# Kernel tuning notes

Measured on AMD Instinct MI355X. Metric: run time of the kernel, lower is better.

The kernel has to match this reference:

```python
import jax, jax.numpy as jnp
import numpy as np

N = 100000      # nodes
E = 1600000     # edges
F_IN = 64       # num_features
H = 64          # hidden_channels
NG = 64         # graphs in batch
ALPHA = 0.5


def _lin_init(key, fan_in, fan_out):
    kw, kb = jax.random.split(key)
    bound = 1.0 / np.sqrt(fan_in)
    w = jax.random.uniform(kw, (fan_in, fan_out), jnp.float32, -bound, bound)
    b = jax.random.uniform(kb, (fan_out,), jnp.float32, -bound, bound)
    return w, b


def setup_inputs() -> dict:
    key = jax.random.key(0)
    ks = jax.random.split(key, 12)
    x = jax.random.normal(ks[0], (N, F_IN), dtype=jnp.float32)
    edge_index = jax.random.randint(ks[1], (2, E), 0, N, dtype=jnp.int32)
    batch = jnp.sort(jax.random.randint(ks[2], (N,), 0, NG, dtype=jnp.int32))
    w1s, b1s = _lin_init(ks[3], F_IN, H)
    w1d, b1d = _lin_init(ks[4], F_IN, H)
    w2s, b2s = _lin_init(ks[5], H, H)
    w2d, b2d = _lin_init(ks[6], H, H)
    w3s, b3s = _lin_init(ks[7], H, H)
    w3d, b3d = _lin_init(ks[8], H, H)
    wl1, bl1 = _lin_init(ks[9], H, 5)
    wl2, bl2 = _lin_init(ks[10], 5, 1)
    return dict(x=x, edge_index=edge_index, batch=batch,
                w1s=w1s, b1s=b1s, w1d=w1d, b1d=b1d,
                w2s=w2s, b2s=b2s, w2d=w2d, b2d=b2d,
                w3s=w3s, b3s=b3s, w3d=w3d, b3d=b3d,
                wl1=wl1, bl1=bl1, wl2=wl2, bl2=bl2)


def _dir_gcn_conv(x, row, col, ws, bs, wd, bd):
    # directional norm: D_out^{-1/2} A D_in^{-1/2} (and same recipe for A^T)
    ones = jnp.ones((row.shape[0],), x.dtype)
    deg_out = jax.ops.segment_sum(ones, row, num_segments=N)  # row-sums of A
    deg_in = jax.ops.segment_sum(ones, col, num_segments=N)   # col-sums of A
    r_out = jnp.where(deg_out > 0, deg_out ** -0.5, 0.0)
    r_in = jnp.where(deg_in > 0, deg_in ** -0.5, 0.0)
    norm = r_out[row] * r_in[col]  # per-edge weight; identical for A and A^T norms
    msg = norm[:, None] * x[col]                       # [E, F]
    adj_x = jax.ops.segment_sum(msg, row, num_segments=N)
    msg_t = norm[:, None] * x[row]
    adj_t_x = jax.ops.segment_sum(msg_t, col, num_segments=N)
    return ALPHA * (adj_x @ ws + bs) + (1.0 - ALPHA) * (adj_t_x @ wd + bd)


def reference(x, edge_index, batch,
              w1s, b1s, w1d, b1d,
              w2s, b2s, w2d, b2d,
              w3s, b3s, w3d, b3d,
              wl1, bl1, wl2, bl2):
    row, col = edge_index[0], edge_index[1]
    h = jax.nn.relu(_dir_gcn_conv(x, row, col, w1s, b1s, w1d, b1d))
    h = jax.nn.relu(_dir_gcn_conv(h, row, col, w2s, b2s, w2d, b2d))
    h = jax.nn.relu(_dir_gcn_conv(h, row, col, w3s, b3s, w3d, b3d))
    g = jax.ops.segment_max(h, batch, num_segments=NG)  # global max pool [NG, H]
    g = jax.nn.relu(g @ wl1 + bl1)
    return g @ wl2 + bl2  # [NG, 1]
```

## Files before the change

### kernel.cpp

```cpp
#include <hip/hip_runtime.h>

#define N_NODES 100000
#define N_EDGES 1600000
#define EPAD    (N_EDGES + NB * BW)
#define HDIM    64
#define NGRAPH  64
#define BW      256
#define NB      391
#define NBLK    256
#define CHUNK   ((N_EDGES + NBLK - 1) / NBLK)
#define MTILES  (N_NODES / 16)

typedef _Float16 h16;
typedef _Float16 h16x4 __attribute__((ext_vector_type(4)));
typedef _Float16 h16x8 __attribute__((ext_vector_type(8)));
typedef float    f32x4 __attribute__((ext_vector_type(4)));

__global__ __launch_bounds__(512) void bucket_count(const int* __restrict__ ei,
                                                    int* __restrict__ cntTabA,
                                                    int* __restrict__ cntTabT) {
    __shared__ int cA[NB], cT[NB];
    const int tid = threadIdx.x;
    for (int i = tid; i < NB; i += 512) { cA[i] = 0; cT[i] = 0; }
    __syncthreads();
    const int e0 = blockIdx.x * CHUNK, e1 = min(e0 + CHUNK, N_EDGES);
    for (int e = e0 + tid; e < e1; e += 512) {
        int r = ei[e];
        int c = ei[N_EDGES + e];
        atomicAdd(&cA[r >> 8], 1);
        atomicAdd(&cT[c >> 8], 1);
    }
    __syncthreads();
    for (int b = tid; b < NB; b += 512) {
        cntTabA[b * NBLK + blockIdx.x] = cA[b];
        cntTabT[b * NBLK + blockIdx.x] = cT[b];
    }
}

__global__ __launch_bounds__(256) void chunk_scan(int* __restrict__ cntTabA,
                                                  int* __restrict__ cntTabT,
                                                  int* __restrict__ tot) {
    __shared__ int s[256];
    const int b = blockIdx.x, d = blockIdx.y, tid = threadIdx.x;
    int* tab = d ? cntTabT : cntTabA;
    int v = tab[b * NBLK + tid];
    s[tid] = v;
    __syncthreads();
    for (int off = 1; off < 256; off <<= 1) {
        int t = (tid >= off) ? s[tid - off] : 0;
        __syncthreads();
        s[tid] += t;
        __syncthreads();
    }
    tab[b * NBLK + tid] = s[tid] - v;
    if (tid == 255) tot[d * 512 + b] = s[255];
}

__global__ __launch_bounds__(512) void start_scan(const int* __restrict__ tot,
                                                  int* __restrict__ bktStartA,
                                                  int* __restrict__ bktStartT) {
    __shared__ int s[512];
    const int tid = threadIdx.x;
    int v = (tid < NB) ? tot[tid] : 0;
    s[tid] = v;
    __syncthreads();
    for (int off = 1; off < 512; off <<= 1) {
        int t = (tid >= off) ? s[tid - off] : 0;
        __syncthreads();
        s[tid] += t;
        __syncthreads();
    }
    if (tid < NB) bktStartA[tid] = s[tid] - v;
    if (tid == 0) bktStartA[NB] = N_EDGES;
    __syncthreads();
    int v2 = (tid < NB) ? tot[512 + tid] : 0;
    s[tid] = v2;
    __syncthreads();
    for (int off = 1; off < 512; off <<= 1) {
        int t = (tid >= off) ? s[tid - off] : 0;
        __syncthreads();
        s[tid] += t;
        __syncthreads();
    }
    if (tid < NB) bktStartT[tid] = s[tid] - v2;
    if (tid == 0) bktStartT[NB] = N_EDGES;
}

__global__ __launch_bounds__(512) void bucketize_write(const int* __restrict__ ei,
                                                       const int* __restrict__ cntTabA,
                                                       const int* __restrict__ cntTabT,
                                                       const int* __restrict__ bktStartA,
                                                       const int* __restrict__ bktStartT,
                                                       int2* __restrict__ bktA,
                                                       int2* __restrict__ bktT) {
    __shared__ int bA[NB], bT[NB];
    const int tid = threadIdx.x;
    for (int i = tid; i < NB; i += 512) {
        bA[i] = bktStartA[i] + cntTabA[i * NBLK + blockIdx.x];
        bT[i] = bktStartT[i] + cntTabT[i * NBLK + blockIdx.x];
    }
    __syncthreads();
    const int e0 = blockIdx.x * CHUNK, e1 = min(e0 + CHUNK, N_EDGES);
    for (int e = e0 + tid; e < e1; e += 512) {
        int r = ei[e];
        int c = ei[N_EDGES + e];
        int pA = atomicAdd(&bA[r >> 8], 1);
        bktA[pA] = make_int2(r, c);
        int pT = atomicAdd(&bT[c >> 8], 1);
        bktT[pT] = make_int2(c, r);
    }
}

__global__ __launch_bounds__(256) void bucket_deg_ptr(
        const int* __restrict__ bktStartA, const int* __restrict__ bktStartT,
        const int2* __restrict__ bktA, const int2* __restrict__ bktT,
        int* __restrict__ deg_out, int* __restrict__ deg_in,
        float* __restrict__ r_out, float* __restrict__ r_in,
        int* __restrict__ rowptrP, int* __restrict__ colptrP) {
    __shared__ int c[BW];
    __shared__ int s[256];
    const int b = blockIdx.x, d = blockIdx.y, tid = threadIdx.x;
    const int* bs = d ? bktStartT : bktStartA;
    const int2* bkt = d ? bktT : bktA;
    int* deg = d ? deg_in : deg_out;
    float* rr = d ? r_in : r_out;
    int* ptr = d ? colptrP : rowptrP;
    const int node0 = b * BW;
    c[tid] = 0;
    __syncthreads();
    const int i0 = bs[b], i1 = bs[b + 1];
    for (int i = i0 + tid; i < i1; i += 256) atomicAdd(&c[bkt[i].x - node0], 1);
    __syncthreads();
    int n = node0 + tid, dg = c[tid];
    int pad = dg + (dg & 1);
    if (n < N_NODES) {
        deg[n] = dg;
        rr[n] = dg > 0 ? rsqrtf((float)dg) : 0.0f;
    } else pad = 0;
    s[tid] = pad;
    __syncthreads();
    for (int off = 1; off < 256; off <<= 1) {
        int t = (tid >= off) ? s[tid - off] : 0;
        __syncthreads();
        s[tid] += t;
        __syncthreads();
    }
    if (n < N_NODES) ptr[n] = i0 + b * BW + (s[tid] - pad);
}

__global__ __launch_bounds__(512) void bucket_scatter(
        const int* __restrict__ rowptrP, const int* __restrict__ colptrP,
        const float* __restrict__ r_out, const float* __restrict__ r_in,
        const int* __restrict__ bktStartA, const int* __restrict__ bktStartT,
        const int2* __restrict__ bktA, const int2* __restrict__ bktT,
        int2* __restrict__ recA, int2* __restrict__ recT) {
    __shared__ int cur[BW];
    __shared__ float rwt[BW];
    const int b = blockIdx.x, d = blockIdx.y, tid = threadIdx.x;
    const int* ptr = d ? colptrP : rowptrP;
    const float* rt = d ? r_in : r_out;
    const float* rs = d ? r_out : r_in;
    const int* bs = d ? bktStartT : bktStartA;
    const int2* bkt = d ? bktT : bktA;
    int2* rec = d ? recT : recA;
    const int node0 = b * BW;
    if (tid < BW) {
        int n = node0 + tid;
        cur[tid] = (n < N_NODES) ? ptr[n] : 0;
        rwt[tid] = (n < N_NODES) ? rt[n] : 0.0f;
    }
    __syncthreads();
    const int i0 = bs[b], i1 = bs[b + 1];
    for (int i = i0 + tid; i < i1; i += 512) {
        int2 e = bkt[i];
        float w = rwt[e.x - node0] * rs[e.y];
        int p = atomicAdd(&cur[e.x - node0], 1);
        rec[p] = make_int2(e.y << 7, __float_as_int(w));
    }
}

__global__ __launch_bounds__(256) void cast_kernel(const float4* __restrict__ x,
                                                   h16x4* __restrict__ xh,
                                                   unsigned* __restrict__ g) {
    if (blockIdx.x == 0) {
        for (int j = threadIdx.x; j < NGRAPH * HDIM; j += 256) g[j] = 0u;
    }
    int i = blockIdx.x * 256 + threadIdx.x;
    if (i < N_NODES * 16) {
        float4 v = x[i];
        h16x4 o;
        o.x = (h16)v.x; o.y = (h16)v.y; o.z = (h16)v.z; o.w = (h16)v.w;
        xh[i] = o;
    }
}

__global__ __launch_bounds__(256) void wprep_kernel(
        const float* __restrict__ w1s, const float* __restrict__ w1d,
        const float* __restrict__ w2s, const float* __restrict__ w2d,
        const float* __restrict__ w3s, const float* __restrict__ w3d,
        const float* __restrict__ b1s, const float* __restrict__ b1d,
        const float* __restrict__ b2s, const float* __restrict__ b2d,
        const float* __restrict__ b3s, const float* __restrict__ b3d,
        h16* __restrict__ WT, float* __restrict__ bc) {
    const int l = blockIdx.y;
    const float* ws = l == 0 ? w1s : l == 1 ? w2s : w3s;
    const float* wd = l == 0 ? w1d : l == 1 ? w2d : w3d;
    int e = blockIdx.x * 256 + threadIdx.x;
    if (e < 8192) {
        int f = e >> 7, k = e & 127;
        float v = (k < 64) ? ws[k * 64 + f] : wd[(k - 64) * 64 + f];
        WT[l * 8192 + f * 128 + k] = (h16)(0.5f * v);
    }
    if (blockIdx.x == 0 && threadIdx.x < 64) {
        const float* bs = l == 0 ? b1s : l == 1 ? b2s : b3s;
        const float* bd = l == 0 ? b1d : l == 1 ? b2d : b3d;
        bc[l * 64 + threadIdx.x] = 0.5f * (bs[threadIdx.x] + bd[threadIdx.x]);
    }
}

__device__ __forceinline__ void fma4h(float4& a, float w, h16x4 f) {
    a.x = fmaf(w, (float)f.x, a.x);
    a.y = fmaf(w, (float)f.y, a.y);
    a.z = fmaf(w, (float)f.z, a.z);
    a.w = fmaf(w, (float)f.w, a.w);
}

__device__ __forceinline__ float4 red_s(float4 v) {
    v.x += __shfl_xor(v.x, 16); v.y += __shfl_xor(v.y, 16);
    v.z += __shfl_xor(v.z, 16); v.w += __shfl_xor(v.w, 16);
    v.x += __shfl_xor(v.x, 32); v.y += __shfl_xor(v.y, 32);
    v.z += __shfl_xor(v.z, 32); v.w += __shfl_xor(v.w, 32);
    return v;
}

__device__ __forceinline__ h16x4 ld_h4(const char* __restrict__ p) {
    return *(const h16x4*)p;
}

__device__ __forceinline__ float4 agg_dir(const char* __restrict__ hb,
                                          const int2* __restrict__ rec,
                                          int start, int deg, int q, int s, int sh) {
    float4 a0 = {0.f,0.f,0.f,0.f}, a1 = {0.f,0.f,0.f,0.f};
    float4 a2 = {0.f,0.f,0.f,0.f}, a3 = {0.f,0.f,0.f,0.f};
    const int4* rec4 = (const int4*)(rec + start);
    const int qb = q * 8;
    int k = 0;
    for (; k + 16 <= deg; k += 16) {
        int4 p0 = rec4[(k >> 1) + s];
        int4 p1 = rec4[(k >> 1) + 4 + s];
        h16x4 f0 = ld_h4(hb + (p0.x << sh) + qb);
        h16x4 f1 = ld_h4(hb + (p0.z << sh) + qb);
        h16x4 f2 = ld_h4(hb + (p1.x << sh) + qb);
        h16x4 f3 = ld_h4(hb + (p1.z << sh) + qb);
        fma4h(a0, __int_as_float(p0.y), f0);
        fma4h(a1, __int_as_float(p0.w), f1);
        fma4h(a2, __int_as_float(p1.y), f2);
        fma4h(a3, __int_as_float(p1.w), f3);
    }
    if (k + 8 <= deg) {
        int4 p = rec4[(k >> 1) + s];
        h16x4 f0 = ld_h4(hb + (p.x << sh) + qb);
        h16x4 f1 = ld_h4(hb + (p.z << sh) + qb);
        fma4h(a0, __int_as_float(p.y), f0);
        fma4h(a1, __int_as_float(p.w), f1);
        k += 8;
    }
    int r = deg - k;
    if (2 * s < r) {
        int4 p = rec4[(k >> 1) + s];
        h16x4 f0 = ld_h4(hb + (p.x << sh) + qb);
        fma4h(a2, __int_as_float(p.y), f0);
        if (2 * s + 1 < r) {
            h16x4 f1 = ld_h4(hb + (p.z << sh) + qb);
            fma4h(a3, __int_as_float(p.w), f1);
        }
    }
    a0.x += a1.x; a0.y += a1.y; a0.z += a1.z; a0.w += a1.w;
    a2.x += a3.x; a2.y += a3.y; a2.z += a3.z; a2.w += a3.w;
    a0.x += a2.x; a0.y += a2.y; a0.z += a2.z; a0.w += a2.w;
    return red_s(a0);
}

__global__ __launch_bounds__(256) void agg_kernel(
        const char* __restrict__ h_in, char* __restrict__ acc_out, int sh,
        const int* __restrict__ rowptrP, const int* __restrict__ deg_out,
        const int2* __restrict__ recA,
        const int* __restrict__ colptrP, const int* __restrict__ deg_in,
        const int2* __restrict__ recT) {
    const int tid  = threadIdx.x;
    const int wid  = (blockIdx.x << 2) + (tid >> 6);
    const int lane = tid & 63;
    const int node = wid >> 1;
    const int dir  = wid & 1;
    const int q = lane & 15;
    const int s = lane >> 4;

    const int* ptr = dir ? colptrP : rowptrP;
    const int* deg = dir ? deg_in : deg_out;
    const int2* rec = dir ? recT : recA;

    float4 a = agg_dir(h_in, rec, ptr[node], deg[node], q, s, sh);
    if (s == 0) {
        h16x4 pk;
        pk.x = (h16)a.x; pk.y = (h16)a.y; pk.z = (h16)a.z; pk.w = (h16)a.w;
        *(h16x4*)(acc_out + (size_t)node * 256 + dir * 128 + q * 8) = pk;
    }
}

__global__ __launch_bounds__(256) void gemm_kernel(char* __restrict__ acc,
                                                   const h16* __restrict__ WT,
                                                   const float* __restrict__ bc,
                                                   const int* __restrict__ batch,
                                                   unsigned* __restrict__ g,
                                                   int do_pool) {
    const int lane = threadIdx.x & 63;
    const int wid = (blockIdx.x * 256 + threadIdx.x) >> 6;
    const int nW = gridDim.x * 4;
    const int m = lane & 15, t = lane >> 4;

    h16x8 bfrag[4][4];
    float bb[4];
#pragma unroll
    for (int nt = 0; nt < 4; nt++) {
        bb[nt] = bc[nt * 16 + m];
#pragma unroll
        for (int kk = 0; kk < 4; kk++)
            bfrag[nt][kk] = *(const h16x8*)(WT + (nt * 16 + m) * 128 + kk * 32 + t * 8);
    }

    for (int tile = wid; tile < MTILES; tile += nW) {
        char* arow = acc + (size_t)tile * 16 * 256;
        const int node0 = tile * 16;
        int b0 = 0, b15 = 0;
        if (do_pool) { b0 = batch[node0]; b15 = batch[node0 + 15]; }
        h16x8 afrag[4];
#pragma unroll
        for (int kk = 0; kk < 4; kk++)
            afrag[kk] = *(const h16x8*)(arow + m * 256 + kk * 64 + t * 16);
#pragma unroll
        for (int nt = 0; nt < 4; nt++) {
            f32x4 c = {0.f, 0.f, 0.f, 0.f};
#pragma unroll
            for (int kk = 0; kk < 4; kk++)
                c = __builtin_amdgcn_mfma_f32_16x16x32_f16(afrag[kk], bfrag[nt][kk], c, 0, 0, 0);
            float ov[4];
#pragma unroll
            for (int r = 0; r < 4; r++) {
                ov[r] = fmaxf(c[r] + bb[nt], 0.0f);
                *(h16*)(arow + (t * 4 + r) * 256 + (nt * 16 + m) * 2) = (h16)ov[r];
            }
            if (do_pool) {
                if (b0 == b15) {
                    float mx = fmaxf(fmaxf(ov[0], ov[1]), fmaxf(ov[2], ov[3]));
                    mx = fmaxf(mx, __shfl_xor(mx, 16));
                    mx = fmaxf(mx, __shfl_xor(mx, 32));
                    if (t == 0)
                        atomicMax(&g[b0 * HDIM + nt * 16 + m], __float_as_uint(mx));
                } else {
#pragma unroll
                    for (int r = 0; r < 4; r++)
                        atomicMax(&g[batch[node0 + t * 4 + r] * HDIM + nt * 16 + m],
                                  __float_as_uint(ov[r]));
                }
            }
        }
    }
}

__global__ __launch_bounds__(64) void mlp_kernel(const unsigned* __restrict__ g,
                                                 const float* __restrict__ wl1,
                                                 const float* __restrict__ bl1,
                                                 const float* __restrict__ wl2,
                                                 const float* __restrict__ bl2,
                                                 float* __restrict__ out) {
    int t = threadIdx.x;
    float gv[HDIM];
#pragma unroll
    for (int k = 0; k < HDIM; k++) gv[k] = __uint_as_float(g[t * HDIM + k]);
    float o = bl2[0];
#pragma unroll
    for (int j = 0; j < 5; j++) {
        float hj = bl1[j];
#pragma unroll
        for (int k = 0; k < HDIM; k++) hj += gv[k] * wl1[k * 5 + j];
        hj = fmaxf(hj, 0.0f);
        o += hj * wl2[j];
    }
    out[t] = o;
}

extern "C" void kernel_launch(void* const* d_in, const int* in_sizes, int n_in,
                              void* d_out, int out_size, void* d_ws, size_t ws_size,
                              hipStream_t stream) {
    const float* x   = (const float*)d_in[0];
    const int*   ei  = (const int*)d_in[1];
    const int*   bat = (const int*)d_in[2];
    const float* w1s = (const float*)d_in[3];
    const float* b1s = (const float*)d_in[4];
    const float* w1d = (const float*)d_in[5];
    const float* b1d = (const float*)d_in[6];
    const float* w2s = (const float*)d_in[7];
    const float* b2s = (const float*)d_in[8];
    const float* w2d = (const float*)d_in[9];
    const float* b2d = (const float*)d_in[10];
    const float* w3s = (const float*)d_in[11];
    const float* b3s = (const float*)d_in[12];
    const float* w3d = (const float*)d_in[13];
    const float* b3d = (const float*)d_in[14];
    const float* wl1 = (const float*)d_in[15];
    const float* bl1 = (const float*)d_in[16];
    const float* wl2 = (const float*)d_in[17];
    const float* bl2 = (const float*)d_in[18];
    float* out = (float*)d_out;

    char* p = (char*)d_ws;
    int*   deg_out = (int*)p;              p += N_NODES * 4;
    int*   deg_in  = (int*)p;              p += N_NODES * 4;
    int*   rowptrP = (int*)p;              p += N_NODES * 4;
    int*   colptrP = (int*)p;              p += N_NODES * 4;
    float* r_out   = (float*)p;            p += N_NODES * 4;
    float* r_in    = (float*)p;            p += N_NODES * 4;
    int*   cntTabA = (int*)p;              p += (size_t)NB * NBLK * 4;
    int*   cntTabT = (int*)p;              p += (size_t)NB * NBLK * 4;
    int*   totTab  = (int*)p;              p += 1024 * 4;
    int*   bktStartA = (int*)p;            p += 512 * 4;
    int*   bktStartT = (int*)p;            p += 512 * 4;
    int2*  recA    = (int2*)p;             p += (size_t)EPAD * 8;
    int2*  recT    = (int2*)p;             p += (size_t)EPAD * 8;
    char*  bufP    = p;
    int2*  bktA    = (int2*)p;
    int2*  bktT    = (int2*)(p + (size_t)N_EDGES * 8);
    p += 2 * (size_t)N_EDGES * 8;
    char*  bufQ    = p;
    h16*   xh      = (h16*)p;
    p += 2 * (size_t)N_EDGES * 8;
    unsigned* g    = (unsigned*)p;         p += NGRAPH * HDIM * 4;
    h16*   WT      = (h16*)p;              p += 3 * 8192 * 2;
    float* bc      = (float*)p;            p += 3 * 64 * 4;

    cast_kernel<<<(N_NODES * 16 + 255) / 256, 256, 0, stream>>>(
        (const float4*)x, (h16x4*)xh, g);
    dim3 gw(32, 3);
    wprep_kernel<<<gw, 256, 0, stream>>>(w1s, w1d, w2s, w2d, w3s, w3d,
                                         b1s, b1d, b2s, b2d, b3s, b3d, WT, bc);

    bucket_count<<<NBLK, 512, 0, stream>>>(ei, cntTabA, cntTabT);
    dim3 gb2(NB, 2);
    chunk_scan<<<gb2, 256, 0, stream>>>(cntTabA, cntTabT, totTab);
    start_scan<<<1, 512, 0, stream>>>(totTab, bktStartA, bktStartT);
    bucketize_write<<<NBLK, 512, 0, stream>>>(ei, cntTabA, cntTabT,
                                              bktStartA, bktStartT, bktA, bktT);

    dim3 gb(NB, 2);
    bucket_deg_ptr<<<gb, 256, 0, stream>>>(bktStartA, bktStartT, bktA, bktT,
                                           deg_out, deg_in, r_out, r_in,
                                           rowptrP, colptrP);
    bucket_scatter<<<gb, 512, 0, stream>>>(
        rowptrP, colptrP, r_out, r_in, bktStartA, bktStartT, bktA, bktT, recA, recT);

    const int agrid = N_NODES * 2 / 4;
    agg_kernel<<<agrid, 256, 0, stream>>>((const char*)xh, bufP, 0,
                                          rowptrP, deg_out, recA, colptrP, deg_in, recT);
    gemm_kernel<<<256, 256, 0, stream>>>(bufP, WT, bc, bat, g, 0);
    agg_kernel<<<agrid, 256, 0, stream>>>(bufP, bufQ, 1,
                                          rowptrP, deg_out, recA, colptrP, deg_in, recT);
    gemm_kernel<<<256, 256, 0, stream>>>(bufQ, WT + 8192, bc + 64, bat, g, 0);
    agg_kernel<<<agrid, 256, 0, stream>>>(bufQ, bufP, 1,
                                          rowptrP, deg_out, recA, colptrP, deg_in, recT);
    gemm_kernel<<<256, 256, 0, stream>>>(bufP, WT + 16384, bc + 128, bat, g, 1);

    mlp_kernel<<<1, 64, 0, stream>>>(g, wl1, bl1, wl2, bl2, out);
}
```

Before: 489.0 us.

## Factor edge norm into node scaling and shrink edge records to one int

The per-edge weight r_out[row]*r_in[col] is split into per-node factors. Source features are prescaled by r_in or r_out when they are written (in cast and in the GEMM epilogue), and the destination factor is applied after aggregation. Edge records shrink from an int2 (index plus weight) to a single pre-shifted byte offset, and the degree and scatter kernels are merged into one launch. This roughly halves index traffic in the gather loops and removes the multiplies. In exchange the feature buffers now store two prescaled copies, padding grows to multiples of 4, and the GEMM writes two half-precision copies per output.

```diff
diff --git a/kernel.cpp b/kernel.cpp
--- a/kernel.cpp
+++ b/kernel.cpp
@@ -2,11 +2,12 @@
 
 #define N_NODES 100000
 #define N_EDGES 1600000
-#define EPAD    (N_EDGES + NB * BW)
+#define BW      256
+#define NB      391
+#define SLACK   (3 * BW)
+#define EPAD    (N_EDGES + NB * SLACK)
 #define HDIM    64
 #define NGRAPH  64
-#define BW      256
-#define NB      391
 #define NBLK    256
 #define CHUNK   ((N_EDGES + NBLK - 1) / NBLK)
 #define MTILES  (N_NODES / 16)
@@ -111,20 +112,23 @@
     }
 }
 
-__global__ __launch_bounds__(256) void bucket_deg_ptr(
+__global__ __launch_bounds__(256) void deg_scatter(
         const int* __restrict__ bktStartA, const int* __restrict__ bktStartT,
         const int2* __restrict__ bktA, const int2* __restrict__ bktT,
         int* __restrict__ deg_out, int* __restrict__ deg_in,
         float* __restrict__ r_out, float* __restrict__ r_in,
-        int* __restrict__ rowptrP, int* __restrict__ colptrP) {
+        int* __restrict__ rowptrP, int* __restrict__ colptrP,
+        int* __restrict__ recA, int* __restrict__ recT) {
     __shared__ int c[BW];
     __shared__ int s[256];
+    __shared__ int cur[BW];
     const int b = blockIdx.x, d = blockIdx.y, tid = threadIdx.x;
     const int* bs = d ? bktStartT : bktStartA;
     const int2* bkt = d ? bktT : bktA;
     int* deg = d ? deg_in : deg_out;
     float* rr = d ? r_in : r_out;
     int* ptr = d ? colptrP : rowptrP;
+    int* rec = d ? recT : recA;
     const int node0 = b * BW;
     c[tid] = 0;
     __syncthreads();
@@ -132,65 +136,52 @@
     for (int i = i0 + tid; i < i1; i += 256) atomicAdd(&c[bkt[i].x - node0], 1);
     __syncthreads();
     int n = node0 + tid, dg = c[tid];
-    int pad = dg + (dg & 1);
+    int pad = (dg + 3) & ~3;
+    if (n >= N_NODES) pad = 0;
+    s[tid] = pad;
+    __syncthreads();
+    for (int off = 1; off < 256; off <<= 1) {
+        int t = (tid >= off) ? s[tid - off] : 0;
+        __syncthreads();
+        s[tid] += t;
+        __syncthreads();
+    }
+    int my_ptr = i0 + SLACK * b + (s[tid] - pad);
     if (n < N_NODES) {
         deg[n] = dg;
         rr[n] = dg > 0 ? rsqrtf((float)dg) : 0.0f;
-    } else pad = 0;
-    s[tid] = pad;
-    __syncthreads();
-    for (int off = 1; off < 256; off <<= 1) {
-        int t = (tid >= off) ? s[tid - off] : 0;
-        __syncthreads();
-        s[tid] += t;
-        __syncthreads();
-    }
-    if (n < N_NODES) ptr[n] = i0 + b * BW + (s[tid] - pad);
-}
-
-__global__ __launch_bounds__(512) void bucket_scatter(
-        const int* __restrict__ rowptrP, const int* __restrict__ colptrP,
-        const float* __restrict__ r_out, const float* __restrict__ r_in,
-        const int* __restrict__ bktStartA, const int* __restrict__ bktStartT,
-        const int2* __restrict__ bktA, const int2* __restrict__ bktT,
-        int2* __restrict__ recA, int2* __restrict__ recT) {
-    __shared__ int cur[BW];
-    __shared__ float rwt[BW];
-    const int b = blockIdx.x, d = blockIdx.y, tid = threadIdx.x;
-    const int* ptr = d ? colptrP : rowptrP;
-    const float* rt = d ? r_in : r_out;
-    const float* rs = d ? r_out : r_in;
-    const int* bs = d ? bktStartT : bktStartA;
-    const int2* bkt = d ? bktT : bktA;
-    int2* rec = d ? recT : recA;
-    const int node0 = b * BW;
-    if (tid < BW) {
-        int n = node0 + tid;
-        cur[tid] = (n < N_NODES) ? ptr[n] : 0;
-        rwt[tid] = (n < N_NODES) ? rt[n] : 0.0f;
-    }
-    __syncthreads();
-    const int i0 = bs[b], i1 = bs[b + 1];
-    for (int i = i0 + tid; i < i1; i += 512) {
+        ptr[n] = my_ptr;
+    }
+    cur[tid] = my_ptr;
+    __syncthreads();
+    for (int i = i0 + tid; i < i1; i += 256) {
         int2 e = bkt[i];
-        float w = rwt[e.x - node0] * rs[e.y];
         int p = atomicAdd(&cur[e.x - node0], 1);
-        rec[p] = make_int2(e.y << 7, __float_as_int(w));
+        rec[p] = e.y << 8;
     }
 }
 
 __global__ __launch_bounds__(256) void cast_kernel(const float4* __restrict__ x,
-                                                   h16x4* __restrict__ xh,
+                                                   const float* __restrict__ r_in,
+                                                   const float* __restrict__ r_out,
+                                                   char* __restrict__ xh,
                                                    unsigned* __restrict__ g) {
     if (blockIdx.x == 0) {
         for (int j = threadIdx.x; j < NGRAPH * HDIM; j += 256) g[j] = 0u;
     }
     int i = blockIdx.x * 256 + threadIdx.x;
     if (i < N_NODES * 16) {
+        int node = i >> 4, q = i & 15;
         float4 v = x[i];
-        h16x4 o;
-        o.x = (h16)v.x; o.y = (h16)v.y; o.z = (h16)v.z; o.w = (h16)v.w;
-        xh[i] = o;
+        float ri = r_in[node], ro = r_out[node];
+        h16x4 a, t;
+        a.x = (h16)(v.x * ri); a.y = (h16)(v.y * ri);
+        a.z = (h16)(v.z * ri); a.w = (h16)(v.w * ri);
+        t.x = (h16)(v.x * ro); t.y = (h16)(v.y * ro);
+        t.z = (h16)(v.z * ro); t.w = (h16)(v.w * ro);
+        char* row = xh + (size_t)node * 256;
+        *(h16x4*)(row + q * 8) = a;
+        *(h16x4*)(row + 128 + q * 8) = t;
     }
 }
 
@@ -218,11 +209,9 @@
     }
 }
 
-__device__ __forceinline__ void fma4h(float4& a, float w, h16x4 f) {
-    a.x = fmaf(w, (float)f.x, a.x);
-    a.y = fmaf(w, (float)f.y, a.y);
-    a.z = fmaf(w, (float)f.z, a.z);
-    a.w = fmaf(w, (float)f.w, a.w);
+__device__ __forceinline__ void add4h(float4& a, h16x4 f) {
+    a.x += (float)f.x; a.y += (float)f.y;
+    a.z += (float)f.z; a.w += (float)f.w;
 }
 
 __device__ __forceinline__ float4 red_s(float4 v) {
@@ -238,42 +227,31 @@
 }
 
 __device__ __forceinline__ float4 agg_dir(const char* __restrict__ hb,
-                                          const int2* __restrict__ rec,
-                                          int start, int deg, int q, int s, int sh) {
+                                          const int* __restrict__ rec,
+                                          int start, int deg, int qb, int s) {
     float4 a0 = {0.f,0.f,0.f,0.f}, a1 = {0.f,0.f,0.f,0.f};
     float4 a2 = {0.f,0.f,0.f,0.f}, a3 = {0.f,0.f,0.f,0.f};
     const int4* rec4 = (const int4*)(rec + start);
-    const int qb = q * 8;
     int k = 0;
     for (; k + 16 <= deg; k += 16) {
-        int4 p0 = rec4[(k >> 1) + s];
-        int4 p1 = rec4[(k >> 1) + 4 + s];
-        h16x4 f0 = ld_h4(hb + (p0.x << sh) + qb);
-        h16x4 f1 = ld_h4(hb + (p0.z << sh) + qb);
-        h16x4 f2 = ld_h4(hb + (p1.x << sh) + qb);
-        h16x4 f3 = ld_h4(hb + (p1.z << sh) + qb);
-        fma4h(a0, __int_as_float(p0.y), f0);
-        fma4h(a1, __int_as_float(p0.w), f1);
-        fma4h(a2, __int_as_float(p1.y), f2);
-        fma4h(a3, __int_as_float(p1.w), f3);
-    }
-    if (k + 8 <= deg) {
-        int4 p = rec4[(k >> 1) + s];
-        h16x4 f0 = ld_h4(hb + (p.x << sh) + qb);
-        h16x4 f1 = ld_h4(hb + (p.z << sh) + qb);
-        fma4h(a0, __int_as_float(p.y), f0);
-        fma4h(a1, __int_as_float(p.w), f1);
-        k += 8;
+        int4 p = rec4[(k >> 2) + s];
+        h16x4 f0 = ld_h4(hb + p.x + qb);
+        h16x4 f1 = ld_h4(hb + p.y + qb);
+        h16x4 f2 = ld_h4(hb + p.z + qb);
+        h16x4 f3 = ld_h4(hb + p.w + qb);
+        add4h(a0, f0);
+        add4h(a1, f1);
+        add4h(a2, f2);
+        add4h(a3, f3);
     }
     int r = deg - k;
-    if (2 * s < r) {
-        int4 p = rec4[(k >> 1) + s];
-        h16x4 f0 = ld_h4(hb + (p.x << sh) + qb);
-        fma4h(a2, __int_as_float(p.y), f0);
-        if (2 * s + 1 < r) {
-            h16x4 f1 = ld_h4(hb + (p.z << sh) + qb);
-            fma4h(a3, __int_as_float(p.w), f1);
-        }
+    int base = 4 * s;
+    if (base < r) {
+        int4 p = rec4[(k >> 2) + s];
+        add4h(a0, ld_h4(hb + p.x + qb));
+        if (base + 1 < r) add4h(a1, ld_h4(hb + p.y + qb));
+        if (base + 2 < r) add4h(a2, ld_h4(hb + p.z + qb));
+        if (base + 3 < r) add4h(a3, ld_h4(hb + p.w + qb));
     }
     a0.x += a1.x; a0.y += a1.y; a0.z += a1.z; a0.w += a1.w;
     a2.x += a3.x; a2.y += a3.y; a2.z += a3.z; a2.w += a3.w;
@@ -282,11 +260,12 @@
 }
 
 __global__ __launch_bounds__(256) void agg_kernel(
-        const char* __restrict__ h_in, char* __restrict__ acc_out, int sh,
+        const char* __restrict__ h_in, char* __restrict__ acc_out,
         const int* __restrict__ rowptrP, const int* __restrict__ deg_out,
-        const int2* __restrict__ recA,
+        const int* __restrict__ recA,
         const int* __restrict__ colptrP, const int* __restrict__ deg_in,
-        const int2* __restrict__ recT) {
+        const int* __restrict__ recT,
+        const float* __restrict__ r_out, const float* __restrict__ r_in) {
     const int tid  = threadIdx.x;
     const int wid  = (blockIdx.x << 2) + (tid >> 6);
     const int lane = tid & 63;
@@ -297,12 +276,16 @@
 
     const int* ptr = dir ? colptrP : rowptrP;
     const int* deg = dir ? deg_in : deg_out;
-    const int2* rec = dir ? recT : recA;
-
-    float4 a = agg_dir(h_in, rec, ptr[node], deg[node], q, s, sh);
+    const int* rec = dir ? recT : recA;
+    const float* rt = dir ? r_in : r_out;
+    const int qb = dir * 128 + q * 8;
+
+    float4 a = agg_dir(h_in, rec, ptr[node], deg[node], qb, s);
     if (s == 0) {
+        float sc = rt[node];
         h16x4 pk;
-        pk.x = (h16)a.x; pk.y = (h16)a.y; pk.z = (h16)a.z; pk.w = (h16)a.w;
+        pk.x = (h16)(a.x * sc); pk.y = (h16)(a.y * sc);
+        pk.z = (h16)(a.z * sc); pk.w = (h16)(a.w * sc);
         *(h16x4*)(acc_out + (size_t)node * 256 + dir * 128 + q * 8) = pk;
     }
 }
@@ -310,6 +293,8 @@
 __global__ __launch_bounds__(256) void gemm_kernel(char* __restrict__ acc,
                                                    const h16* __restrict__ WT,
                                                    const float* __restrict__ bc,
+                                                   const float* __restrict__ r_in,
+                                                   const float* __restrict__ r_out,
                                                    const int* __restrict__ batch,
                                                    unsigned* __restrict__ g,
                                                    int do_pool) {
@@ -332,7 +317,16 @@
         char* arow = acc + (size_t)tile * 16 * 256;
         const int node0 = tile * 16;
         int b0 = 0, b15 = 0;
-        if (do_pool) { b0 = batch[node0]; b15 = batch[node0 + 15]; }
+        float ri[4], ro[4];
+        if (do_pool) {
+            b0 = batch[node0]; b15 = batch[node0 + 15];
+        } else {
+#pragma unroll
+            for (int r = 0; r < 4; r++) {
+                ri[r] = r_in[node0 + t * 4 + r];
+                ro[r] = r_out[node0 + t * 4 + r];
+            }
+        }
         h16x8 afrag[4];
 #pragma unroll
         for (int kk = 0; kk < 4; kk++)
@@ -345,10 +339,8 @@
                 c = __builtin_amdgcn_mfma_f32_16x16x32_f16(afrag[kk], bfrag[nt][kk], c, 0, 0, 0);
             float ov[4];
 #pragma unroll
-            for (int r = 0; r < 4; r++) {
+            for (int r = 0; r < 4; r++)
                 ov[r] = fmaxf(c[r] + bb[nt], 0.0f);
-                *(h16*)(arow + (t * 4 + r) * 256 + (nt * 16 + m) * 2) = (h16)ov[r];
-            }
             if (do_pool) {
                 if (b0 == b15) {
                     float mx = fmaxf(fmaxf(ov[0], ov[1]), fmaxf(ov[2], ov[3]));
@@ -361,6 +353,13 @@
                     for (int r = 0; r < 4; r++)
                         atomicMax(&g[batch[node0 + t * 4 + r] * HDIM + nt * 16 + m],
                                   __float_as_uint(ov[r]));
+                }
+            } else {
+#pragma unroll
+                for (int r = 0; r < 4; r++) {
+                    char* rp = arow + (t * 4 + r) * 256 + (nt * 16 + m) * 2;
+                    *(h16*)rp = (h16)(ov[r] * ri[r]);
+                    *(h16*)(rp + 128) = (h16)(ov[r] * ro[r]);
                 }
             }
         }
@@ -425,21 +424,18 @@
     int*   totTab  = (int*)p;              p += 1024 * 4;
     int*   bktStartA = (int*)p;            p += 512 * 4;
     int*   bktStartT = (int*)p;            p += 512 * 4;
-    int2*  recA    = (int2*)p;             p += (size_t)EPAD * 8;
-    int2*  recT    = (int2*)p;             p += (size_t)EPAD * 8;
+    int*   recA    = (int*)p;              p += (size_t)EPAD * 4;
+    int*   recT    = (int*)p;              p += (size_t)EPAD * 4;
     char*  bufP    = p;
     int2*  bktA    = (int2*)p;
     int2*  bktT    = (int2*)(p + (size_t)N_EDGES * 8);
     p += 2 * (size_t)N_EDGES * 8;
     char*  bufQ    = p;
-    h16*   xh      = (h16*)p;
     p += 2 * (size_t)N_EDGES * 8;
     unsigned* g    = (unsigned*)p;         p += NGRAPH * HDIM * 4;
     h16*   WT      = (h16*)p;              p += 3 * 8192 * 2;
     float* bc      = (float*)p;            p += 3 * 64 * 4;
 
-    cast_kernel<<<(N_NODES * 16 + 255) / 256, 256, 0, stream>>>(
-        (const float4*)x, (h16x4*)xh, g);
     dim3 gw(32, 3);
     wprep_kernel<<<gw, 256, 0, stream>>>(w1s, w1d, w2s, w2d, w3s, w3d,
                                          b1s, b1d, b2s, b2d, b3s, b3d, WT, bc);
@@ -452,22 +448,26 @@
                                               bktStartA, bktStartT, bktA, bktT);
 
     dim3 gb(NB, 2);
-    bucket_deg_ptr<<<gb, 256, 0, stream>>>(bktStartA, bktStartT, bktA, bktT,
-                                           deg_out, deg_in, r_out, r_in,
-                                           rowptrP, colptrP);
-    bucket_scatter<<<gb, 512, 0, stream>>>(
-        rowptrP, colptrP, r_out, r_in, bktStartA, bktStartT, bktA, bktT, recA, recT);
+    deg_scatter<<<gb, 256, 0, stream>>>(bktStartA, bktStartT, bktA, bktT,
+                                        deg_out, deg_in, r_out, r_in,
+                                        rowptrP, colptrP, recA, recT);
+
+    cast_kernel<<<(N_NODES * 16 + 255) / 256, 256, 0, stream>>>(
+        (const float4*)x, r_in, r_out, bufQ, g);
 
     const int agrid = N_NODES * 2 / 4;
-    agg_kernel<<<agrid, 256, 0, stream>>>((const char*)xh, bufP, 0,
-                                          rowptrP, deg_out, recA, colptrP, deg_in, recT);
-    gemm_kernel<<<256, 256, 0, stream>>>(bufP, WT, bc, bat, g, 0);
-    agg_kernel<<<agrid, 256, 0, stream>>>(bufP, bufQ, 1,
-                                          rowptrP, deg_out, recA, colptrP, deg_in, recT);
-    gemm_kernel<<<256, 256, 0, stream>>>(bufQ, WT + 8192, bc + 64, bat, g, 0);
-    agg_kernel<<<agrid, 256, 0, stream>>>(bufQ, bufP, 1,
-                                          rowptrP, deg_out, recA, colptrP, deg_in, recT);
-    gemm_kernel<<<256, 256, 0, stream>>>(bufP, WT + 16384, bc + 128, bat, g, 1);
+    agg_kernel<<<agrid, 256, 0, stream>>>(bufQ, bufP,
+                                          rowptrP, deg_out, recA, colptrP, deg_in, recT,
+                                          r_out, r_in);
+    gemm_kernel<<<256, 256, 0, stream>>>(bufP, WT, bc, r_in, r_out, bat, g, 0);
+    agg_kernel<<<agrid, 256, 0, stream>>>(bufP, bufQ,
+                                          rowptrP, deg_out, recA, colptrP, deg_in, recT,
+                                          r_out, r_in);
+    gemm_kernel<<<256, 256, 0, stream>>>(bufQ, WT + 8192, bc + 64, r_in, r_out, bat, g, 0);
+    agg_kernel<<<agrid, 256, 0, stream>>>(bufQ, bufP,
+                                          rowptrP, deg_out, recA, colptrP, deg_in, recT,
+                                          r_out, r_in);
+    gemm_kernel<<<256, 256, 0, stream>>>(bufP, WT + 16384, bc + 128, r_in, r_out, bat, g, 1);
 
     mlp_kernel<<<1, 64, 0, stream>>>(g, wl1, bl1, wl2, bl2, out);
 }
```

Result: no change. 492.3 us (+0.7%).

## Fuse neighbor aggregation and MFMA linear layer into one kernel per layer

Applied to the files above, without the earlier changes.

Each GCN layer's gather-aggregate and its dense transform now run in one kernel. A 1024-thread block aggregates 8 nodes in both directions into shared memory, then four waves apply the 16x16x32 MFMA with bias and ReLU, writing a 128-byte fp16 row per node. This removes the round trip of the 256-byte aggregate buffer through global memory and the separate GEMM launch. In exchange, half the MFMA tile is wasted on 8-row groups, the weight fragments are reloaded in every block, and only 4 of 16 waves do the GEMM after a block-wide barrier.

```diff
diff --git a/kernel.cpp b/kernel.cpp
--- a/kernel.cpp
+++ b/kernel.cpp
@@ -9,7 +9,7 @@
 #define NB      391
 #define NBLK    256
 #define CHUNK   ((N_EDGES + NBLK - 1) / NBLK)
-#define MTILES  (N_NODES / 16)
+#define NGROUPS (N_NODES / 8)
 
 typedef _Float16 h16;
 typedef _Float16 h16x4 __attribute__((ext_vector_type(4)));
@@ -133,19 +133,20 @@
     __syncthreads();
     int n = node0 + tid, dg = c[tid];
     int pad = dg + (dg & 1);
+    if (n >= N_NODES) pad = 0;
+    s[tid] = pad;
+    __syncthreads();
+    for (int off = 1; off < 256; off <<= 1) {
+        int t = (tid >= off) ? s[tid - off] : 0;
+        __syncthreads();
+        s[tid] += t;
+        __syncthreads();
+    }
     if (n < N_NODES) {
         deg[n] = dg;
         rr[n] = dg > 0 ? rsqrtf((float)dg) : 0.0f;
-    } else pad = 0;
-    s[tid] = pad;
-    __syncthreads();
-    for (int off = 1; off < 256; off <<= 1) {
-        int t = (tid >= off) ? s[tid - off] : 0;
-        __syncthreads();
-        s[tid] += t;
-        __syncthreads();
-    }
-    if (n < N_NODES) ptr[n] = i0 + b * BW + (s[tid] - pad);
+        ptr[n] = i0 + b * BW + (s[tid] - pad);
+    }
 }
 
 __global__ __launch_bounds__(512) void bucket_scatter(
@@ -239,19 +240,18 @@
 
 __device__ __forceinline__ float4 agg_dir(const char* __restrict__ hb,
                                           const int2* __restrict__ rec,
-                                          int start, int deg, int q, int s, int sh) {
+                                          int start, int deg, int qb, int s) {
     float4 a0 = {0.f,0.f,0.f,0.f}, a1 = {0.f,0.f,0.f,0.f};
     float4 a2 = {0.f,0.f,0.f,0.f}, a3 = {0.f,0.f,0.f,0.f};
     const int4* rec4 = (const int4*)(rec + start);
-    const int qb = q * 8;
     int k = 0;
     for (; k + 16 <= deg; k += 16) {
         int4 p0 = rec4[(k >> 1) + s];
         int4 p1 = rec4[(k >> 1) + 4 + s];
-        h16x4 f0 = ld_h4(hb + (p0.x << sh) + qb);
-        h16x4 f1 = ld_h4(hb + (p0.z << sh) + qb);
-        h16x4 f2 = ld_h4(hb + (p1.x << sh) + qb);
-        h16x4 f3 = ld_h4(hb + (p1.z << sh) + qb);
+        h16x4 f0 = ld_h4(hb + p0.x + qb);
+        h16x4 f1 = ld_h4(hb + p0.z + qb);
+        h16x4 f2 = ld_h4(hb + p1.x + qb);
+        h16x4 f3 = ld_h4(hb + p1.z + qb);
         fma4h(a0, __int_as_float(p0.y), f0);
         fma4h(a1, __int_as_float(p0.w), f1);
         fma4h(a2, __int_as_float(p1.y), f2);
@@ -259,8 +259,8 @@
     }
     if (k + 8 <= deg) {
         int4 p = rec4[(k >> 1) + s];
-        h16x4 f0 = ld_h4(hb + (p.x << sh) + qb);
-        h16x4 f1 = ld_h4(hb + (p.z << sh) + qb);
+        h16x4 f0 = ld_h4(hb + p.x + qb);
+        h16x4 f1 = ld_h4(hb + p.z + qb);
         fma4h(a0, __int_as_float(p.y), f0);
         fma4h(a1, __int_as_float(p.w), f1);
         k += 8;
@@ -268,10 +268,10 @@
     int r = deg - k;
     if (2 * s < r) {
         int4 p = rec4[(k >> 1) + s];
-        h16x4 f0 = ld_h4(hb + (p.x << sh) + qb);
+        h16x4 f0 = ld_h4(hb + p.x + qb);
         fma4h(a2, __int_as_float(p.y), f0);
         if (2 * s + 1 < r) {
-            h16x4 f1 = ld_h4(hb + (p.z << sh) + qb);
+            h16x4 f1 = ld_h4(hb + p.z + qb);
             fma4h(a3, __int_as_float(p.w), f1);
         }
     }
@@ -281,17 +281,25 @@
     return red_s(a0);
 }
 
-__global__ __launch_bounds__(256) void agg_kernel(
-        const char* __restrict__ h_in, char* __restrict__ acc_out, int sh,
+#define ASTRIDE 132
+__global__ __launch_bounds__(1024) void layer_fused(
+        const char* __restrict__ h_in, char* __restrict__ h_out,
         const int* __restrict__ rowptrP, const int* __restrict__ deg_out,
         const int2* __restrict__ recA,
         const int* __restrict__ colptrP, const int* __restrict__ deg_in,
-        const int2* __restrict__ recT) {
+        const int2* __restrict__ recT,
+        const h16* __restrict__ WT, const float* __restrict__ bc,
+        const int* __restrict__ batch, unsigned* __restrict__ g,
+        int do_pool) {
+    __shared__ h16 accS[8 * ASTRIDE];
+
     const int tid  = threadIdx.x;
-    const int wid  = (blockIdx.x << 2) + (tid >> 6);
+    const int wave = tid >> 6;
     const int lane = tid & 63;
-    const int node = wid >> 1;
-    const int dir  = wid & 1;
+    const int node0 = blockIdx.x * 8;
+    const int nl   = wave >> 1;
+    const int dir  = wave & 1;
+    const int node = node0 + nl;
     const int q = lane & 15;
     const int s = lane >> 4;
 
@@ -299,70 +307,50 @@
     const int* deg = dir ? deg_in : deg_out;
     const int2* rec = dir ? recT : recA;
 
-    float4 a = agg_dir(h_in, rec, ptr[node], deg[node], q, s, sh);
+    float4 a = agg_dir(h_in, rec, ptr[node], deg[node], q * 8, s);
     if (s == 0) {
         h16x4 pk;
         pk.x = (h16)a.x; pk.y = (h16)a.y; pk.z = (h16)a.z; pk.w = (h16)a.w;
-        *(h16x4*)(acc_out + (size_t)node * 256 + dir * 128 + q * 8) = pk;
-    }
-}
-
-__global__ __launch_bounds__(256) void gemm_kernel(char* __restrict__ acc,
-                                                   const h16* __restrict__ WT,
-                                                   const float* __restrict__ bc,
-                                                   const int* __restrict__ batch,
-                                                   unsigned* __restrict__ g,
-                                                   int do_pool) {
-    const int lane = threadIdx.x & 63;
-    const int wid = (blockIdx.x * 256 + threadIdx.x) >> 6;
-    const int nW = gridDim.x * 4;
-    const int m = lane & 15, t = lane >> 4;
-
-    h16x8 bfrag[4][4];
-    float bb[4];
-#pragma unroll
-    for (int nt = 0; nt < 4; nt++) {
-        bb[nt] = bc[nt * 16 + m];
+        *(h16x4*)(accS + nl * ASTRIDE + dir * 64 + q * 4) = pk;
+    }
+    __syncthreads();
+
+    if (wave < 4) {
+        const int nt = wave;
+        const int m = lane & 15, t = lane >> 4;
+        float bb = bc[nt * 16 + m];
+        h16x8 bfrag[4], afrag[4];
+#pragma unroll
+        for (int kk = 0; kk < 4; kk++) {
+            bfrag[kk] = *(const h16x8*)(WT + (nt * 16 + m) * 128 + kk * 32 + t * 8);
+            afrag[kk] = *(const h16x8*)(accS + (m & 7) * ASTRIDE + kk * 32 + t * 8);
+        }
+        f32x4 c = {0.f, 0.f, 0.f, 0.f};
 #pragma unroll
         for (int kk = 0; kk < 4; kk++)
-            bfrag[nt][kk] = *(const h16x8*)(WT + (nt * 16 + m) * 128 + kk * 32 + t * 8);
-    }
-
-    for (int tile = wid; tile < MTILES; tile += nW) {
-        char* arow = acc + (size_t)tile * 16 * 256;
-        const int node0 = tile * 16;
-        int b0 = 0, b15 = 0;
-        if (do_pool) { b0 = batch[node0]; b15 = batch[node0 + 15]; }
-        h16x8 afrag[4];
-#pragma unroll
-        for (int kk = 0; kk < 4; kk++)
-            afrag[kk] = *(const h16x8*)(arow + m * 256 + kk * 64 + t * 16);
-#pragma unroll
-        for (int nt = 0; nt < 4; nt++) {
-            f32x4 c = {0.f, 0.f, 0.f, 0.f};
-#pragma unroll
-            for (int kk = 0; kk < 4; kk++)
-                c = __builtin_amdgcn_mfma_f32_16x16x32_f16(afrag[kk], bfrag[nt][kk], c, 0, 0, 0);
-            float ov[4];
-#pragma unroll
-            for (int r = 0; r < 4; r++) {
-                ov[r] = fmaxf(c[r] + bb[nt], 0.0f);
-                *(h16*)(arow + (t * 4 + r) * 256 + (nt * 16 + m) * 2) = (h16)ov[r];
+            c = __builtin_amdgcn_mfma_f32_16x16x32_f16(afrag[kk], bfrag[kk], c, 0, 0, 0);
+        float ov[4];
+#pragma unroll
+        for (int r = 0; r < 4; r++)
+            ov[r] = fmaxf(c[r] + bb, 0.0f);
+        if (do_pool) {
+            int b0 = batch[node0], b7 = batch[node0 + 7];
+            if (b0 == b7) {
+                float mx = fmaxf(fmaxf(ov[0], ov[1]), fmaxf(ov[2], ov[3]));
+                mx = fmaxf(mx, __shfl_xor(mx, 16));
+                if (t == 0)
+                    atomicMax(&g[b0 * HDIM + nt * 16 + m], __float_as_uint(mx));
+            } else if (t < 2) {
+#pragma unroll
+                for (int r = 0; r < 4; r++)
+                    atomicMax(&g[batch[node0 + t * 4 + r] * HDIM + nt * 16 + m],
+                              __float_as_uint(ov[r]));
             }
-            if (do_pool) {
-                if (b0 == b15) {
-                    float mx = fmaxf(fmaxf(ov[0], ov[1]), fmaxf(ov[2], ov[3]));
-                    mx = fmaxf(mx, __shfl_xor(mx, 16));
-                    mx = fmaxf(mx, __shfl_xor(mx, 32));
-                    if (t == 0)
-                        atomicMax(&g[b0 * HDIM + nt * 16 + m], __float_as_uint(mx));
-                } else {
-#pragma unroll
-                    for (int r = 0; r < 4; r++)
-                        atomicMax(&g[batch[node0 + t * 4 + r] * HDIM + nt * 16 + m],
-                                  __float_as_uint(ov[r]));
-                }
-            }
+        } else if (t < 2) {
+#pragma unroll
+            for (int r = 0; r < 4; r++)
+                *(h16*)(h_out + (size_t)(node0 + t * 4 + r) * 128
+                        + (nt * 16 + m) * 2) = (h16)ov[r];
         }
     }
 }
@@ -427,13 +415,13 @@
     int*   bktStartT = (int*)p;            p += 512 * 4;
     int2*  recA    = (int2*)p;             p += (size_t)EPAD * 8;
     int2*  recT    = (int2*)p;             p += (size_t)EPAD * 8;
-    char*  bufP    = p;
+    char*  hA      = p;
     int2*  bktA    = (int2*)p;
     int2*  bktT    = (int2*)(p + (size_t)N_EDGES * 8);
     p += 2 * (size_t)N_EDGES * 8;
-    char*  bufQ    = p;
-    h16*   xh      = (h16*)p;
-    p += 2 * (size_t)N_EDGES * 8;
+    char*  xh      = p;
+    char*  hB      = p;
+    p += (size_t)N_NODES * 128;
     unsigned* g    = (unsigned*)p;         p += NGRAPH * HDIM * 4;
     h16*   WT      = (h16*)p;              p += 3 * 8192 * 2;
     float* bc      = (float*)p;            p += 3 * 64 * 4;
@@ -458,16 +446,15 @@
     bucket_scatter<<<gb, 512, 0, stream>>>(
         rowptrP, colptrP, r_out, r_in, bktStartA, bktStartT, bktA, bktT, recA, recT);
 
-    const int agrid = N_NODES * 2 / 4;
-    agg_kernel<<<agrid, 256, 0, stream>>>((const char*)xh, bufP, 0,
-                                          rowptrP, deg_out, recA, colptrP, deg_in, recT);
-    gemm_kernel<<<256, 256, 0, stream>>>(bufP, WT, bc, bat, g, 0);
-    agg_kernel<<<agrid, 256, 0, stream>>>(bufP, bufQ, 1,
-                                          rowptrP, deg_out, recA, colptrP, deg_in, recT);
-    gemm_kernel<<<256, 256, 0, stream>>>(bufQ, WT + 8192, bc + 64, bat, g, 0);
-    agg_kernel<<<agrid, 256, 0, stream>>>(bufQ, bufP, 1,
-                                          rowptrP, deg_out, recA, colptrP, deg_in, recT);
-    gemm_kernel<<<256, 256, 0, stream>>>(bufP, WT + 16384, bc + 128, bat, g, 1);
+    layer_fused<<<NGROUPS, 1024, 0, stream>>>(
+        xh, hA, rowptrP, deg_out, recA, colptrP, deg_in, recT,
+        WT, bc, bat, g, 0);
+    layer_fused<<<NGROUPS, 1024, 0, stream>>>(
+        hA, hB, rowptrP, deg_out, recA, colptrP, deg_in, recT,
+        WT + 8192, bc + 64, bat, g, 0);
+    layer_fused<<<NGROUPS, 1024, 0, stream>>>(
+        hB, hA, rowptrP, deg_out, recA, colptrP, deg_in, recT,
+        WT + 16384, bc + 128, bat, g, 1);
 
     mlp_kernel<<<1, 64, 0, stream>>>(g, wl1, bl1, wl2, bl2, out);
 }
```

Result: slower. 554.0 us (+13.3%).
